# Optimization experiments

Hardware: AMD Instinct MI355X
Metric: run time of the kernel (lower is better)

## Reference

```python
import jax, jax.numpy as jnp
import numpy as np

B, S = 2, 512
HID, FEAT = 768, 256
H, W = 512, 512
NUM_CLASSES = 9
BN_EPS = 1e-5


def setup_inputs() -> dict:
    key = jax.random.key(0)
    ks = jax.random.split(key, 20)
    hidden_states = jax.random.normal(ks[0], (B, S, HID), dtype=jnp.float32)
    # bbox in LayoutLM 0..1000 space, guaranteed x2>x1, y2>y1 for realistic coverage
    x1 = jax.random.randint(ks[1], (B, S), 0, 880)
    y1 = jax.random.randint(ks[2], (B, S), 0, 880)
    bw = jax.random.randint(ks[3], (B, S), 8, 120)
    bh = jax.random.randint(ks[4], (B, S), 8, 120)
    bbox = jnp.stack([x1, y1, jnp.minimum(x1 + bw, 1000), jnp.minimum(y1 + bh, 1000)], axis=-1).astype(jnp.int32)
    attention_mask = jnp.ones((B, S), dtype=jnp.int32)
    w_init = lambda k, shp: jax.random.normal(k, shp, dtype=jnp.float32) * 0.02
    return {
        "hidden_states": hidden_states,
        "bbox": bbox,
        "attention_mask": attention_mask,
        "proj_w": w_init(ks[5], (HID, FEAT)),
        "proj_b": jnp.zeros((FEAT,), jnp.float32),
        "conv1_w": w_init(ks[6], (128, FEAT, 3, 3)),
        "conv1_b": jnp.zeros((128,), jnp.float32),
        "bn1_g": jnp.ones((128,), jnp.float32),
        "bn1_b": jnp.zeros((128,), jnp.float32),
        "bn1_m": jnp.zeros((128,), jnp.float32),
        "bn1_v": jnp.ones((128,), jnp.float32),
        "conv2_w": w_init(ks[7], (64, 128, 3, 3)),
        "conv2_b": jnp.zeros((64,), jnp.float32),
        "bn2_g": jnp.ones((64,), jnp.float32),
        "bn2_b": jnp.zeros((64,), jnp.float32),
        "bn2_m": jnp.zeros((64,), jnp.float32),
        "bn2_v": jnp.ones((64,), jnp.float32),
        "conv3_w": w_init(ks[8], (NUM_CLASSES, 64, 1, 1)),
        "conv3_b": jnp.zeros((NUM_CLASSES,), jnp.float32),
    }


def _conv(x, w, b, pad):
    y = jax.lax.conv_general_dilated(x, w, (1, 1), [(pad, pad), (pad, pad)],
                                     dimension_numbers=("NCHW", "OIHW", "NCHW"))
    return y + b[None, :, None, None]


def _bn(x, g, b, m, v):
    scale = g / jnp.sqrt(v + BN_EPS)
    return (x - m[None, :, None, None]) * scale[None, :, None, None] + b[None, :, None, None]


def reference(hidden_states, bbox, attention_mask, proj_w, proj_b,
              conv1_w, conv1_b, bn1_g, bn1_b, bn1_m, bn1_v,
              conv2_w, conv2_b, bn2_g, bn2_b, bn2_m, bn2_v,
              conv3_w, conv3_b):
    features = hidden_states @ proj_w + proj_b  # [B,S,FEAT]

    # integer pixel coords, matching int(x * dim / 1000) truncation for x >= 0
    x1 = jnp.maximum((bbox[..., 0] * W) // 1000, 0)
    y1 = jnp.maximum((bbox[..., 1] * H) // 1000, 0)
    x2 = jnp.minimum((bbox[..., 2] * W) // 1000, W - 1)
    y2 = jnp.minimum((bbox[..., 3] * H) // 1000, H - 1)
    valid = (attention_mask == 1) & (jnp.arange(S) >= 1) & (x2 > x1) & (y2 > y1)  # [B,S]

    rows = jnp.arange(H)
    cols = jnp.arange(W)
    rows_in = (rows[None, None, :] >= y1[..., None]) & (rows[None, None, :] < y2[..., None])  # [B,S,H]
    cols_in = (cols[None, None, :] >= x1[..., None]) & (cols[None, None, :] < x2[..., None])  # [B,S,W]

    # sequential priority scatter: later tokens overwrite earlier ones
    def step(winner, xs):
        r, c, v, i = xs  # r:[B,H] c:[B,W] v:[B] i:scalar
        cov = v[:, None, None] & (r[:, :, None] & c[:, None, :])
        return jnp.where(cov, i, winner), None

    winner0 = jnp.zeros((B, H, W), jnp.int32)  # 0 == empty (token 0 is never valid)
    xs = (rows_in.transpose(1, 0, 2), cols_in.transpose(1, 0, 2),
          valid.T, jnp.arange(S, dtype=jnp.int32))
    winner, _ = jax.lax.scan(step, winner0, xs)  # [B,H,W]

    idx = winner.reshape(B, H * W)
    fm = jnp.take_along_axis(features, idx[:, :, None], axis=1)  # [B,HW,FEAT]
    fm = jnp.where((idx > 0)[:, :, None], fm, 0.0)
    feature_map = fm.reshape(B, H, W, FEAT).transpose(0, 3, 1, 2)  # [B,FEAT,H,W]

    x = jax.nn.relu(_bn(_conv(feature_map, conv1_w, conv1_b, 1), bn1_g, bn1_b, bn1_m, bn1_v))
    x = jax.nn.relu(_bn(_conv(x, conv2_w, conv2_b, 1), bn2_g, bn2_b, bn2_m, bn2_v))
    logits = _conv(x, conv3_w, conv3_b, 0)  # [B,NUM_CLASSES,H,W]
    return logits
```

## Files before the change

### kernel.cpp

```cpp
#include <hip/hip_runtime.h>
#include <hip/hip_bf16.h>

typedef __bf16 bf16x8 __attribute__((ext_vector_type(8)));
typedef float f32x4 __attribute__((ext_vector_type(4)));

#define HH 512
#define WW 512
#define NC 9
#define LDSB 16896
#define SCRATCH_OFF 0
#define W3_OFF 33792
#define B3_OFF 36096

static __device__ __forceinline__ ushort f2bf(float x) {
  union { float f; unsigned u; } c; c.f = x;
  unsigned r = c.u + 0x7FFFu + ((c.u >> 16) & 1u);
  return (ushort)(r >> 16);
}

__global__ __launch_bounds__(256) void proj_gemm_kernel(
    const float* __restrict__ hs, const float* __restrict__ pw,
    const float* __restrict__ pb, float* __restrict__ feat) {
  __shared__ float As[16 * 132];
  __shared__ float4 Bs4[2048];
  int tid = threadIdx.x;
  int r0 = blockIdx.x * 16;
  int n0 = blockIdx.y * 64;
  int r = tid >> 4;
  int c4 = (tid & 15) << 2;
  float4 acc = *(const float4*)(pb + n0 + c4);
  for (int k0 = 0; k0 < 768; k0 += 128) {
    __syncthreads();
    #pragma unroll
    for (int i = 0; i < 8; ++i) {
      int idx = tid + i * 256;
      As[(idx >> 7) * 132 + (idx & 127)] =
          hs[(size_t)(r0 + (idx >> 7)) * 768 + k0 + (idx & 127)];
    }
    #pragma unroll
    for (int i = 0; i < 8; ++i) {
      int idx = tid + i * 256;
      Bs4[idx] = *(const float4*)(pw + (size_t)(k0 + (idx >> 4)) * 256 + n0 + ((idx & 15) << 2));
    }
    __syncthreads();
    const float* ar = As + r * 132;
    #pragma unroll 8
    for (int k = 0; k < 128; ++k) {
      float a = ar[k];
      float4 bv = Bs4[(k << 4) + (c4 >> 2)];
      acc.x = fmaf(a, bv.x, acc.x); acc.y = fmaf(a, bv.y, acc.y);
      acc.z = fmaf(a, bv.z, acc.z); acc.w = fmaf(a, bv.w, acc.w);
    }
  }
  *(float4*)(feat + (size_t)(r0 + r) * 256 + n0 + c4) = acc;
}

__global__ __launch_bounds__(64) void scatter_kernel(
    const int* __restrict__ bbox, const int* __restrict__ amask,
    int* __restrict__ winner) {
  int token = blockIdx.x;
  int b = token >> 9, s = token & 511;
  if (s == 0) return;
  const int* bb = bbox + (size_t)token * 4;
  int x1 = (bb[0] * 512) / 1000; if (x1 < 0) x1 = 0;
  int y1 = (bb[1] * 512) / 1000; if (y1 < 0) y1 = 0;
  int x2 = (bb[2] * 512) / 1000; if (x2 > 511) x2 = 511;
  int y2 = (bb[3] * 512) / 1000; if (y2 > 511) y2 = 511;
  if (amask[token] != 1 || x2 <= x1 || y2 <= y1) return;
  int lane = threadIdx.x;
  for (int yy = y1; yy < y2; ++yy) {
    int rowbase = (b << 18) + (yy << 9);
    for (int xx = x1 + lane; xx < x2; xx += 64)
      atomicMax(&winner[rowbase + xx], s);
  }
}

__global__ __launch_bounds__(256) void w1r_kernel(
    const float* __restrict__ w1, float* __restrict__ w1r) {
  int idx = blockIdx.x * 256 + threadIdx.x;
  int ic = idx / 1152, rem = idx - ic * 1152;
  int tap = rem >> 7, oc = rem & 127;
  w1r[idx] = w1[(size_t)oc * 2304 + ic * 9 + tap];
}

__global__ __launch_bounds__(256) void gtab_gemm_kernel(
    const float* __restrict__ feat, const float* __restrict__ w1r,
    float* __restrict__ G) {
  __shared__ float As[16 * 132];
  __shared__ float4 Bs4[2048];
  int tid = threadIdx.x;
  int r0 = blockIdx.x * 16;
  int n0 = blockIdx.y * 64;
  int r = tid >> 4;
  int c4 = (tid & 15) << 2;
  float4 acc = make_float4(0.f, 0.f, 0.f, 0.f);
  for (int k0 = 0; k0 < 256; k0 += 128) {
    __syncthreads();
    #pragma unroll
    for (int i = 0; i < 8; ++i) {
      int idx = tid + i * 256;
      As[(idx >> 7) * 132 + (idx & 127)] =
          feat[(size_t)(r0 + (idx >> 7)) * 256 + k0 + (idx & 127)];
    }
    #pragma unroll
    for (int i = 0; i < 8; ++i) {
      int idx = tid + i * 256;
      Bs4[idx] = *(const float4*)(w1r + (size_t)(k0 + (idx >> 4)) * 1152 + n0 + ((idx & 15) << 2));
    }
    __syncthreads();
    const float* ar = As + r * 132;
    #pragma unroll 8
    for (int k = 0; k < 128; ++k) {
      float a = ar[k];
      float4 bv = Bs4[(k << 4) + (c4 >> 2)];
      acc.x = fmaf(a, bv.x, acc.x); acc.y = fmaf(a, bv.y, acc.y);
      acc.z = fmaf(a, bv.z, acc.z); acc.w = fmaf(a, bv.w, acc.w);
    }
  }
  int row = r0 + r;
  if ((row & 511) == 0) acc = make_float4(0.f, 0.f, 0.f, 0.f);
  *(float4*)(G + (size_t)row * 1152 + n0 + c4) = acc;
}

__global__ __launch_bounds__(256) void gall_kernel(
    const float* __restrict__ G, float* __restrict__ Gall) {
  int idx = blockIdx.x * 256 + threadIdx.x;
  int row = idx >> 7, oc = idx & 127;
  const float* gr = G + (size_t)row * 1152 + oc;
  float s = 0.f;
  #pragma unroll
  for (int t = 0; t < 9; ++t) s += gr[t * 128];
  Gall[idx] = s;
}

__global__ __launch_bounds__(256) void w2t_kernel(
    const float* __restrict__ w2, ushort* __restrict__ w2t) {
  int oc = blockIdx.x;
  for (int k = threadIdx.x; k < 1152; k += 256) {
    int tap = k >> 7, ic = k & 127;
    w2t[(size_t)oc * 1152 + k] = f2bf(w2[(size_t)oc * 1152 + ic * 9 + tap]);
  }
}

__global__ __launch_bounds__(256) void conv1_gather_kernel(
    const int* __restrict__ winner,
    const float* __restrict__ G, const float* __restrict__ Gall,
    const float* __restrict__ cb, const float* __restrict__ g,
    const float* __restrict__ bt, const float* __restrict__ m,
    const float* __restrict__ v,
    ushort* __restrict__ buf1, int b, int hstart) {
  __shared__ float sscl[128], sshf[128];
  int tid = threadIdx.x;
  if (tid < 128) {
    float s = g[tid] * rsqrtf(v[tid] + 1e-5f);
    sscl[tid] = s;
    sshf[tid] = (cb[tid] - m[tid]) * s + bt[tid];
  }
  __syncthreads();
  int px = blockIdx.x * 256 + tid;
  int r = px >> 9, w = px & 511;
  int h = hstart + r;
  ushort* dst = buf1 + (size_t)px * 128;
  if (h < 0 || h >= HH) {
    uint4 z = make_uint4(0, 0, 0, 0);
    #pragma unroll
    for (int j = 0; j < 16; ++j) *(uint4*)(dst + j * 8) = z;
    return;
  }
  const int* wb = winner + (b << 18);
  int win[9];
  #pragma unroll
  for (int ky = 0; ky < 3; ++ky)
    #pragma unroll
    for (int kx = 0; kx < 3; ++kx) {
      int hp = h - 1 + ky, wp = w - 1 + kx;
      int s = 0;
      if (hp >= 0 && hp < HH && wp >= 0 && wp < WW) s = wb[(hp << 9) + wp];
      win[ky * 3 + kx] = s;
    }
  bool alleq = true;
  #pragma unroll
  for (int t = 1; t < 9; ++t) alleq = alleq && (win[t] == win[0]);

  if (alleq) {
    const float4* gp = (const float4*)(Gall + ((((size_t)b << 9) + win[0]) << 7));
    #pragma unroll
    for (int o8 = 0; o8 < 16; ++o8) {
      float4 a0 = gp[o8 * 2], a1 = gp[o8 * 2 + 1];
      const float* sc = &sscl[o8 * 8];
      const float* sh = &sshf[o8 * 8];
      union { ushort us[8]; uint4 v4; } pk;
      pk.us[0] = f2bf(fmaxf(fmaf(a0.x, sc[0], sh[0]), 0.f));
      pk.us[1] = f2bf(fmaxf(fmaf(a0.y, sc[1], sh[1]), 0.f));
      pk.us[2] = f2bf(fmaxf(fmaf(a0.z, sc[2], sh[2]), 0.f));
      pk.us[3] = f2bf(fmaxf(fmaf(a0.w, sc[3], sh[3]), 0.f));
      pk.us[4] = f2bf(fmaxf(fmaf(a1.x, sc[4], sh[4]), 0.f));
      pk.us[5] = f2bf(fmaxf(fmaf(a1.y, sc[5], sh[5]), 0.f));
      pk.us[6] = f2bf(fmaxf(fmaf(a1.z, sc[6], sh[6]), 0.f));
      pk.us[7] = f2bf(fmaxf(fmaf(a1.w, sc[7], sh[7]), 0.f));
      *(uint4*)(dst + o8 * 8) = pk.v4;
    }
  } else {
    size_t off[9];
    #pragma unroll
    for (int t = 0; t < 9; ++t)
      off[t] = ((size_t)((b << 9) + win[t])) * 1152 + t * 128;
    #pragma unroll
    for (int o8 = 0; o8 < 16; ++o8) {
      float4 a0 = make_float4(0, 0, 0, 0), a1 = a0;
      #pragma unroll
      for (int t = 0; t < 9; ++t) {
        const float4* gp = (const float4*)(G + off[t] + o8 * 8);
        float4 g0 = gp[0], g1 = gp[1];
        a0.x += g0.x; a0.y += g0.y; a0.z += g0.z; a0.w += g0.w;
        a1.x += g1.x; a1.y += g1.y; a1.z += g1.z; a1.w += g1.w;
      }
      const float* sc = &sscl[o8 * 8];
      const float* sh = &sshf[o8 * 8];
      union { ushort us[8]; uint4 v4; } pk;
      pk.us[0] = f2bf(fmaxf(fmaf(a0.x, sc[0], sh[0]), 0.f));
      pk.us[1] = f2bf(fmaxf(fmaf(a0.y, sc[1], sh[1]), 0.f));
      pk.us[2] = f2bf(fmaxf(fmaf(a0.z, sc[2], sh[2]), 0.f));
      pk.us[3] = f2bf(fmaxf(fmaf(a0.w, sc[3], sh[3]), 0.f));
      pk.us[4] = f2bf(fmaxf(fmaf(a1.x, sc[4], sh[4]), 0.f));
      pk.us[5] = f2bf(fmaxf(fmaf(a1.y, sc[5], sh[5]), 0.f));
      pk.us[6] = f2bf(fmaxf(fmaf(a1.z, sc[6], sh[6]), 0.f));
      pk.us[7] = f2bf(fmaxf(fmaf(a1.w, sc[7], sh[7]), 0.f));
      *(uint4*)(dst + o8 * 8) = pk.v4;
    }
  }
}

__global__ __launch_bounds__(256) void conv2_mfma_kernel(
    const ushort* __restrict__ buf1, const ushort* __restrict__ w2t,
    const float* __restrict__ cb, const float* __restrict__ g,
    const float* __restrict__ bt, const float* __restrict__ m_,
    const float* __restrict__ v_,
    const float* __restrict__ w3, const float* __restrict__ b3,
    float* __restrict__ out, int b, int hs0, int SR) {
  __shared__ uint4 lds4[3360];
  char* smem = (char*)lds4;
  int tid = threadIdx.x;
  int w0 = blockIdx.x * 64;
  int oh0 = blockIdx.y * 2;
  int wave = tid >> 6, lane = tid & 63;
  int wavem = wave >> 1, waven = wave & 1;
  int l15 = lane & 15, l4 = lane >> 4;

  float scl[2], shf[2];
  #pragma unroll
  for (int nf = 0; nf < 2; ++nf) {
    int oc = waven * 32 + nf * 16 + l15;
    float s = g[oc] * rsqrtf(v_[oc] + 1e-5f);
    scl[nf] = s;
    shf[nf] = (cb[oc] - m_[oc]) * s + bt[oc];
  }

  int aaddr[4][3];
  #pragma unroll
  for (int mf = 0; mf < 4; ++mf)
    #pragma unroll
    for (int kx = 0; kx < 3; ++kx) {
      int col = mf * 16 + l15 + kx;
      aaddr[mf][kx] = wavem * 4224 + (col << 6) + ((l4 << 4) ^ (((col >> 1) & 3) << 4));
    }
  int baddr[2];
  #pragma unroll
  for (int nf = 0; nf < 2; ++nf) {
    int n = waven * 32 + nf * 16 + l15;
    baddr[nf] = LDSB + (n << 6) + ((l4 << 4) ^ (((n >> 1) & 3) << 4));
  }

  f32x4 acc[4][2];
  #pragma unroll
  for (int mf = 0; mf < 4; ++mf)
    #pragma unroll
    for (int nf = 0; nf < 2; ++nf)
      acc[mf][nf] = (f32x4){0.f, 0.f, 0.f, 0.f};

  int bn = tid >> 2, bslot = tid & 3;
  int bd = LDSB + (bn << 6) + ((bslot << 4) ^ (((bn >> 1) & 3) << 4));

  for (int chunk = 0; chunk < 4; ++chunk) {
    int ic0 = chunk * 32;
    __syncthreads();
    uint4 av0, av1, av2, av3, av4;
    int ad0, ad1, ad2, ad3, ad4 = 0;
    av4 = make_uint4(0, 0, 0, 0);
#define ADEC(II, AV, AD) { \
      int i_ = (II); int slot = i_ & 3; int q = i_ >> 2; \
      int r_ = (q * 993) >> 16; int c_ = q - r_ * 66; \
      int wg = w0 - 1 + c_; \
      AD = ((r_ * 66 + c_) << 6) + ((slot << 4) ^ (((c_ >> 1) & 3) << 4)); \
      AV = make_uint4(0, 0, 0, 0); \
      if (wg >= 0 && wg < 512) \
        AV = *(const uint4*)(buf1 + ((((size_t)(oh0 + r_)) << 9) + wg) * 128 + ic0 + slot * 8); \
    }
    ADEC(tid, av0, ad0);
    ADEC(tid + 256, av1, ad1);
    ADEC(tid + 512, av2, ad2);
    ADEC(tid + 768, av3, ad3);
    if (tid < 32) ADEC(tid + 1024, av4, ad4);
#undef ADEC
    uint4 bv[9];
    const ushort* wsrc = w2t + (size_t)bn * 1152 + ic0 + bslot * 8;
    #pragma unroll
    for (int j = 0; j < 9; ++j) bv[j] = *(const uint4*)(wsrc + j * 128);

    *(uint4*)(smem + ad0) = av0;
    *(uint4*)(smem + ad1) = av1;
    *(uint4*)(smem + ad2) = av2;
    *(uint4*)(smem + ad3) = av3;
    if (tid < 32) *(uint4*)(smem + ad4) = av4;
    #pragma unroll
    for (int j = 0; j < 9; ++j) *(uint4*)(smem + bd + j * 4096) = bv[j];
    __syncthreads();

    #pragma unroll
    for (int ky = 0; ky < 3; ++ky) {
      #pragma unroll
      for (int kx = 0; kx < 3; ++kx) {
        const int tap = ky * 3 + kx;
        bf16x8 bf0 = *(const bf16x8*)(smem + baddr[0] + tap * 4096);
        bf16x8 bf1 = *(const bf16x8*)(smem + baddr[1] + tap * 4096);
        #pragma unroll
        for (int mf = 0; mf < 4; ++mf) {
          bf16x8 af = *(const bf16x8*)(smem + aaddr[mf][kx] + ky * 4224);
          acc[mf][0] = __builtin_amdgcn_mfma_f32_16x16x32_bf16(af, bf0, acc[mf][0], 0, 0, 0);
          acc[mf][1] = __builtin_amdgcn_mfma_f32_16x16x32_bf16(af, bf1, acc[mf][1], 0, 0, 0);
        }
      }
    }
  }

  __syncthreads();
  #pragma unroll
  for (int mf = 0; mf < 4; ++mf)
    #pragma unroll
    for (int nf = 0; nf < 2; ++nf)
      #pragma unroll
      for (int rr = 0; rr < 4; ++rr) {
        int mm = wavem * 64 + mf * 16 + l4 * 4 + rr;
        int oc = waven * 32 + nf * 16 + l15;
        float val = fmaxf(fmaf(acc[mf][nf][rr], scl[nf], shf[nf]), 0.f);
        *(float*)(smem + SCRATCH_OFF + (mm * 66 + oc) * 4) = val;
      }
  if (tid >= 128) {
    int idx = tid - 128;
    #pragma unroll
    for (int j = 0; j < 2; ++j) {
      int ii = idx + j * 128;
      if (ii < 144) *(uint4*)(smem + W3_OFF + ii * 16) = *(const uint4*)(w3 + ii * 4);
    }
    if (idx < NC) *(float*)(smem + B3_OFF + idx * 4) = b3[idx];
  }
  __syncthreads();

  if (tid < 128) {
    int px = tid;
    const float* w3f = (const float*)(smem + W3_OFF);
    const float* b3f = (const float*)(smem + B3_OFF);
    float a9[NC];
    #pragma unroll
    for (int c = 0; c < NC; ++c) a9[c] = b3f[c];
    #pragma unroll 8
    for (int j = 0; j < 32; ++j) {
      float2 xv = *(const float2*)(smem + SCRATCH_OFF + (px * 66 + 2 * j) * 4);
      #pragma unroll
      for (int c = 0; c < NC; ++c)
        a9[c] = fmaf(xv.x, w3f[c * 64 + 2 * j], fmaf(xv.y, w3f[c * 64 + 2 * j + 1], a9[c]));
    }
    int h = hs0 + oh0 + (px >> 6);
    int w = w0 + (px & 63);
    size_t base = ((size_t)b * NC) * 262144 + (size_t)h * 512 + w;
    #pragma unroll
    for (int c = 0; c < NC; ++c) out[base + (size_t)c * 262144] = a9[c];
  }
}

extern "C" void kernel_launch(void* const* d_in, const int* in_sizes, int n_in,
                              void* d_out, int out_size, void* d_ws, size_t ws_size,
                              hipStream_t stream) {
  const float* hs  = (const float*)d_in[0];
  const int* bbox  = (const int*)d_in[1];
  const int* amask = (const int*)d_in[2];
  const float* pw  = (const float*)d_in[3];
  const float* pb  = (const float*)d_in[4];
  const float* w1  = (const float*)d_in[5];
  const float* c1b = (const float*)d_in[6];
  const float* g1  = (const float*)d_in[7];
  const float* b1  = (const float*)d_in[8];
  const float* m1  = (const float*)d_in[9];
  const float* v1  = (const float*)d_in[10];
  const float* w2  = (const float*)d_in[11];
  const float* c2b = (const float*)d_in[12];
  const float* g2  = (const float*)d_in[13];
  const float* b2  = (const float*)d_in[14];
  const float* m2  = (const float*)d_in[15];
  const float* v2  = (const float*)d_in[16];
  const float* w3  = (const float*)d_in[17];
  const float* b3  = (const float*)d_in[18];
  float* out = (float*)d_out;

  char* wsb = (char*)d_ws;
  float*  feat   = (float*)(wsb + 0);
  int*    winner = (int*)(wsb + 1048576);
  float*  G      = (float*)(wsb + 3145728);
  float*  Gall   = (float*)(wsb + 7864320);
  float*  w1r    = (float*)(wsb + 8388608);
  ushort* w2t    = (ushort*)(wsb + 10485760);
  ushort* buf1   = (ushort*)(wsb + 10747904);

  int SR = 512;
  while (SR > 32) {
    size_t need = 10747904 + (size_t)(SR + 2) * 131072;
    if (need <= ws_size) break;
    SR >>= 1;
  }

  hipMemsetAsync(winner, 0, 2097152, stream);
  proj_gemm_kernel<<<dim3(64, 4), 256, 0, stream>>>(hs, pw, pb, feat);
  scatter_kernel<<<1024, 64, 0, stream>>>(bbox, amask, winner);
  w1r_kernel<<<1152, 256, 0, stream>>>(w1, w1r);
  gtab_gemm_kernel<<<dim3(64, 18), 256, 0, stream>>>(feat, w1r, G);
  gall_kernel<<<512, 256, 0, stream>>>(G, Gall);
  w2t_kernel<<<64, 256, 0, stream>>>(w2, w2t);

  int nstripes = 512 / SR;
  for (int b = 0; b < 2; ++b) {
    for (int s = 0; s < nstripes; ++s) {
      int hs0 = s * SR;
      conv1_gather_kernel<<<dim3((SR + 2) * 512 / 256), 256, 0, stream>>>(
          winner, G, Gall, c1b, g1, b1, m1, v1, buf1, b, hs0 - 1);
      conv2_mfma_kernel<<<dim3(8, SR / 2), 256, 0, stream>>>(
          buf1, w2t, c2b, g2, b2, m2, v2, w3, b3, out, b, hs0, SR);
    }
  }
}
```

Before: 285.3 us.

## Double-buffer conv2 activations in LDS, load weights to registers, batch both images

The conv2 MFMA kernel now keeps bf16 weight fragments in registers, read directly from global memory, instead of staging them in LDS. Activation chunks are double-buffered in LDS: the next chunk is prefetched into registers while MFMAs run, which leaves one barrier per chunk. When the workspace allows, both batch images are processed in a single launch of conv1 and conv2 using blockIdx.z. The aim is to cut barrier and LDS traffic, overlap global loads with compute, and remove per-batch launch overhead, at the cost of more VGPRs (18 weight fragments) and possibly lower occupancy.

```diff
diff --git a/kernel.cpp b/kernel.cpp
--- a/kernel.cpp
+++ b/kernel.cpp
@@ -7,10 +7,10 @@
 #define HH 512
 #define WW 512
 #define NC 9
-#define LDSB 16896
-#define SCRATCH_OFF 0
 #define W3_OFF 33792
 #define B3_OFF 36096
+
+#define BARRIER() asm volatile("s_waitcnt lgkmcnt(0)\n\ts_barrier" ::: "memory")
 
 static __device__ __forceinline__ ushort f2bf(float x) {
   union { float f; unsigned u; } c; c.f = x;
@@ -148,7 +148,7 @@
     const float* __restrict__ cb, const float* __restrict__ g,
     const float* __restrict__ bt, const float* __restrict__ m,
     const float* __restrict__ v,
-    ushort* __restrict__ buf1, int b, int hstart) {
+    ushort* __restrict__ buf1, size_t bstride, int b0, int hstart) {
   __shared__ float sscl[128], sshf[128];
   int tid = threadIdx.x;
   if (tid < 128) {
@@ -157,10 +157,11 @@
     sshf[tid] = (cb[tid] - m[tid]) * s + bt[tid];
   }
   __syncthreads();
+  int b = b0 + blockIdx.z;
   int px = blockIdx.x * 256 + tid;
   int r = px >> 9, w = px & 511;
   int h = hstart + r;
-  ushort* dst = buf1 + (size_t)px * 128;
+  ushort* dst = buf1 + (size_t)blockIdx.z * bstride + (size_t)px * 128;
   if (h < 0 || h >= HH) {
     uint4 z = make_uint4(0, 0, 0, 0);
     #pragma unroll
@@ -237,12 +238,14 @@
     const float* __restrict__ bt, const float* __restrict__ m_,
     const float* __restrict__ v_,
     const float* __restrict__ w3, const float* __restrict__ b3,
-    float* __restrict__ out, int b, int hs0, int SR) {
-  __shared__ uint4 lds4[3360];
-  char* smem = (char*)lds4;
+    float* __restrict__ out, int b0, size_t bstride, int hs0) {
+  __shared__ char smem[36160];
   int tid = threadIdx.x;
   int w0 = blockIdx.x * 64;
   int oh0 = blockIdx.y * 2;
+  int bz = blockIdx.z;
+  int b = b0 + bz;
+  const ushort* B1 = buf1 + (size_t)bz * bstride;
   int wave = tid >> 6, lane = tid & 63;
   int wavem = wave >> 1, waven = wave & 1;
   int l15 = lane & 15, l4 = lane >> 4;
@@ -264,11 +267,22 @@
       int col = mf * 16 + l15 + kx;
       aaddr[mf][kx] = wavem * 4224 + (col << 6) + ((l4 << 4) ^ (((col >> 1) & 3) << 4));
     }
-  int baddr[2];
-  #pragma unroll
-  for (int nf = 0; nf < 2; ++nf) {
-    int n = waven * 32 + nf * 16 + l15;
-    baddr[nf] = LDSB + (n << 6) + ((l4 << 4) ^ (((n >> 1) & 3) << 4));
+  const ushort* bbase[2];
+  #pragma unroll
+  for (int nf = 0; nf < 2; ++nf)
+    bbase[nf] = w2t + (size_t)(waven * 32 + nf * 16 + l15) * 1152 + l4 * 8;
+
+  unsigned goff[5]; int ldso[5]; bool act[5], inr[5];
+  #pragma unroll
+  for (int i = 0; i < 5; ++i) {
+    int ii = tid + i * 256;
+    act[i] = (i < 4) || (tid < 32);
+    int slot = ii & 3, q = ii >> 2;
+    int r_ = (q * 993) >> 16, c_ = q - r_ * 66;
+    int wg = w0 - 1 + c_;
+    ldso[i] = ((r_ * 66 + c_) << 6) + ((slot << 4) ^ (((c_ >> 1) & 3) << 4));
+    inr[i] = act[i] && (wg >= 0) && (wg < 512);
+    goff[i] = ((unsigned)((oh0 + r_) << 9) + (unsigned)(wg < 0 ? 0 : wg)) * 128 + slot * 8;
   }
 
   f32x4 acc[4][2];
@@ -278,62 +292,54 @@
     for (int nf = 0; nf < 2; ++nf)
       acc[mf][nf] = (f32x4){0.f, 0.f, 0.f, 0.f};
 
-  int bn = tid >> 2, bslot = tid & 3;
-  int bd = LDSB + (bn << 6) + ((bslot << 4) ^ (((bn >> 1) & 3) << 4));
-
-  for (int chunk = 0; chunk < 4; ++chunk) {
-    int ic0 = chunk * 32;
-    __syncthreads();
-    uint4 av0, av1, av2, av3, av4;
-    int ad0, ad1, ad2, ad3, ad4 = 0;
-    av4 = make_uint4(0, 0, 0, 0);
-#define ADEC(II, AV, AD) { \
-      int i_ = (II); int slot = i_ & 3; int q = i_ >> 2; \
-      int r_ = (q * 993) >> 16; int c_ = q - r_ * 66; \
-      int wg = w0 - 1 + c_; \
-      AD = ((r_ * 66 + c_) << 6) + ((slot << 4) ^ (((c_ >> 1) & 3) << 4)); \
-      AV = make_uint4(0, 0, 0, 0); \
-      if (wg >= 0 && wg < 512) \
-        AV = *(const uint4*)(buf1 + ((((size_t)(oh0 + r_)) << 9) + wg) * 128 + ic0 + slot * 8); \
-    }
-    ADEC(tid, av0, ad0);
-    ADEC(tid + 256, av1, ad1);
-    ADEC(tid + 512, av2, ad2);
-    ADEC(tid + 768, av3, ad3);
-    if (tid < 32) ADEC(tid + 1024, av4, ad4);
-#undef ADEC
-    uint4 bv[9];
-    const ushort* wsrc = w2t + (size_t)bn * 1152 + ic0 + bslot * 8;
-    #pragma unroll
-    for (int j = 0; j < 9; ++j) bv[j] = *(const uint4*)(wsrc + j * 128);
-
-    *(uint4*)(smem + ad0) = av0;
-    *(uint4*)(smem + ad1) = av1;
-    *(uint4*)(smem + ad2) = av2;
-    *(uint4*)(smem + ad3) = av3;
-    if (tid < 32) *(uint4*)(smem + ad4) = av4;
-    #pragma unroll
-    for (int j = 0; j < 9; ++j) *(uint4*)(smem + bd + j * 4096) = bv[j];
-    __syncthreads();
-
+  #pragma unroll
+  for (int i = 0; i < 5; ++i) {
+    uint4 vv = make_uint4(0, 0, 0, 0);
+    if (inr[i]) vv = *(const uint4*)(B1 + goff[i]);
+    if (act[i]) *(uint4*)(smem + ldso[i]) = vv;
+  }
+
+  #pragma unroll
+  for (int c = 0; c < 4; ++c) {
+    const int CUR = (c & 1) ? 16896 : 0;
+    const int NXT = (c & 1) ? 0 : 16896;
+    const int ic0 = c * 32;
+    bf16x8 bf[2][9];
+    #pragma unroll
+    for (int nf = 0; nf < 2; ++nf)
+      #pragma unroll
+      for (int t = 0; t < 9; ++t)
+        bf[nf][t] = *(const bf16x8*)(bbase[nf] + t * 128 + ic0);
+    uint4 av[5];
+    if (c < 3) {
+      #pragma unroll
+      for (int i = 0; i < 5; ++i) {
+        av[i] = make_uint4(0, 0, 0, 0);
+        if (inr[i]) av[i] = *(const uint4*)(B1 + goff[i] + ic0 + 32);
+      }
+    }
+    BARRIER();
     #pragma unroll
     for (int ky = 0; ky < 3; ++ky) {
       #pragma unroll
       for (int kx = 0; kx < 3; ++kx) {
         const int tap = ky * 3 + kx;
-        bf16x8 bf0 = *(const bf16x8*)(smem + baddr[0] + tap * 4096);
-        bf16x8 bf1 = *(const bf16x8*)(smem + baddr[1] + tap * 4096);
         #pragma unroll
         for (int mf = 0; mf < 4; ++mf) {
-          bf16x8 af = *(const bf16x8*)(smem + aaddr[mf][kx] + ky * 4224);
-          acc[mf][0] = __builtin_amdgcn_mfma_f32_16x16x32_bf16(af, bf0, acc[mf][0], 0, 0, 0);
-          acc[mf][1] = __builtin_amdgcn_mfma_f32_16x16x32_bf16(af, bf1, acc[mf][1], 0, 0, 0);
+          bf16x8 af = *(const bf16x8*)(smem + CUR + aaddr[mf][kx] + ky * 4224);
+          acc[mf][0] = __builtin_amdgcn_mfma_f32_16x16x32_bf16(af, bf[0][tap], acc[mf][0], 0, 0, 0);
+          acc[mf][1] = __builtin_amdgcn_mfma_f32_16x16x32_bf16(af, bf[1][tap], acc[mf][1], 0, 0, 0);
         }
       }
     }
-  }
-
-  __syncthreads();
+    if (c < 3) {
+      #pragma unroll
+      for (int i = 0; i < 5; ++i)
+        if (act[i]) *(uint4*)(smem + NXT + ldso[i]) = av[i];
+    }
+  }
+
+  BARRIER();
   #pragma unroll
   for (int mf = 0; mf < 4; ++mf)
     #pragma unroll
@@ -343,7 +349,7 @@
         int mm = wavem * 64 + mf * 16 + l4 * 4 + rr;
         int oc = waven * 32 + nf * 16 + l15;
         float val = fmaxf(fmaf(acc[mf][nf][rr], scl[nf], shf[nf]), 0.f);
-        *(float*)(smem + SCRATCH_OFF + (mm * 66 + oc) * 4) = val;
+        *(float*)(smem + (mm * 66 + oc) * 4) = val;
       }
   if (tid >= 128) {
     int idx = tid - 128;
@@ -354,7 +360,7 @@
     }
     if (idx < NC) *(float*)(smem + B3_OFF + idx * 4) = b3[idx];
   }
-  __syncthreads();
+  BARRIER();
 
   if (tid < 128) {
     int px = tid;
@@ -365,7 +371,7 @@
     for (int c = 0; c < NC; ++c) a9[c] = b3f[c];
     #pragma unroll 8
     for (int j = 0; j < 32; ++j) {
-      float2 xv = *(const float2*)(smem + SCRATCH_OFF + (px * 66 + 2 * j) * 4);
+      float2 xv = *(const float2*)(smem + (px * 66 + 2 * j) * 4);
       #pragma unroll
       for (int c = 0; c < NC; ++c)
         a9[c] = fmaf(xv.x, w3f[c * 64 + 2 * j], fmaf(xv.y, w3f[c * 64 + 2 * j + 1], a9[c]));
@@ -413,10 +419,11 @@
 
   int SR = 512;
   while (SR > 32) {
-    size_t need = 10747904 + (size_t)(SR + 2) * 131072;
-    if (need <= ws_size) break;
+    if (10747904 + (size_t)(SR + 2) * 131072 <= ws_size) break;
     SR >>= 1;
   }
+  size_t b1s = (size_t)(SR + 2) * 65536;
+  int NB = (SR == 512 && ws_size >= 10747904 + 4 * b1s) ? 2 : 1;
 
   hipMemsetAsync(winner, 0, 2097152, stream);
   proj_gemm_kernel<<<dim3(64, 4), 256, 0, stream>>>(hs, pw, pb, feat);
@@ -426,14 +433,21 @@
   gall_kernel<<<512, 256, 0, stream>>>(G, Gall);
   w2t_kernel<<<64, 256, 0, stream>>>(w2, w2t);
 
-  int nstripes = 512 / SR;
-  for (int b = 0; b < 2; ++b) {
-    for (int s = 0; s < nstripes; ++s) {
-      int hs0 = s * SR;
-      conv1_gather_kernel<<<dim3((SR + 2) * 512 / 256), 256, 0, stream>>>(
-          winner, G, Gall, c1b, g1, b1, m1, v1, buf1, b, hs0 - 1);
-      conv2_mfma_kernel<<<dim3(8, SR / 2), 256, 0, stream>>>(
-          buf1, w2t, c2b, g2, b2, m2, v2, w3, b3, out, b, hs0, SR);
-    }
-  }
-}
+  if (NB == 2) {
+    conv1_gather_kernel<<<dim3(1028, 1, 2), 256, 0, stream>>>(
+        winner, G, Gall, c1b, g1, b1, m1, v1, buf1, b1s, 0, -1);
+    conv2_mfma_kernel<<<dim3(8, 256, 2), 256, 0, stream>>>(
+        buf1, w2t, c2b, g2, b2, m2, v2, w3, b3, out, 0, b1s, 0);
+  } else {
+    int nstripes = 512 / SR;
+    for (int b = 0; b < 2; ++b) {
+      for (int s = 0; s < nstripes; ++s) {
+        int hs0 = s * SR;
+        conv1_gather_kernel<<<dim3((SR + 2) * 512 / 256, 1, 1), 256, 0, stream>>>(
+            winner, G, Gall, c1b, g1, b1, m1, v1, buf1, b1s, b, hs0 - 1);
+        conv2_mfma_kernel<<<dim3(8, SR / 2, 1), 256, 0, stream>>>(
+            buf1, w2t, c2b, g2, b2, m2, v2, w3, b3, out, b, b1s, hs0);
+      }
+    }
+  }
+}
```

Result: slower. 358.2 us (+25.5%).
